# Performance work log

Measured on AMD Instinct MI355X. Metric: run time of the kernel, lower is better.

The kernel has to match this reference:

```python
import jax, jax.numpy as jnp
import numpy as np

B, C_IN, H, W = 8, 768, 64, 64
C_OUT = 768
C_QK = C_OUT // 8   # 96
C_V = C_OUT // 8    # 96


def setup_inputs() -> dict:
    key = jax.random.key(0)
    k0, k1, k2, k3, k4 = jax.random.split(key, 5)
    scale = 0.05
    return {
        "x": jax.random.normal(k0, (B, C_IN, H, W), jnp.float32),
        "Wq": jax.random.normal(k1, (C_QK, C_IN), jnp.float32) * scale,
        "Wk": jax.random.normal(k2, (C_QK, C_IN), jnp.float32) * scale,
        "Wv": jax.random.normal(k3, (C_V, C_IN), jnp.float32) * scale,
        "Wlast": jax.random.normal(k4, (C_OUT, C_V), jnp.float32) * scale,
        "gamma": jnp.ones((1,), jnp.float32),
    }


def reference(x, Wq, Wk, Wv, Wlast, gamma):
    # 1x1 convs == channel contractions; produce channels-last [B, H, W, C]
    q = jnp.einsum('bchw,oc->bhwo', x, Wq)   # [B, H, W, Cqk]
    k = jnp.einsum('bchw,oc->bhwo', x, Wk)   # [B, H, W, Cqk]
    v = jnp.einsum('bchw,oc->bhwo', x, Wv)   # [B, H, W, Cv]

    b, h, w, cq = q.shape
    L = h * w
    qf = q.reshape(b, L, cq)
    kf = k.reshape(b, L, cq)
    vf = v.reshape(b, L, v.shape[-1])

    # Unscaled full softmax attention over all spatial positions (batched).
    scores = jnp.einsum('bqc,bkc->bqk', qf, kf)        # [B, L, L]
    beta = jax.nn.softmax(scores, axis=-1)
    out = jnp.einsum('bqk,bkc->bqc', beta, vf)          # [B, L, Cv]
    out = out.reshape(b, h, w, -1)

    # last 1x1 conv (Cv -> C_OUT), scale by gamma, residual add
    y = jnp.einsum('bhwc,oc->bohw', out, Wlast)         # [B, C_OUT, H, W]
    return gamma[0] * y + x
```

## Files before the change

kernel.cpp:

```cpp
#include <hip/hip_runtime.h>

#define NB    8
#define CIN   768
#define LSP   4096
#define DD    96
#define COUT_ 768

typedef __attribute__((ext_vector_type(4))) float f32x4;
typedef __attribute__((ext_vector_type(8))) __bf16 bf16x8;
typedef __attribute__((ext_vector_type(8))) unsigned short us8;
typedef __attribute__((ext_vector_type(4))) unsigned short us4;

static __device__ __forceinline__ unsigned short f2bf(float f){
  union{float f; unsigned u;} v; v.f=f;
  unsigned r = v.u + 0x7FFFu + ((v.u>>16)&1u);
  return (unsigned short)(r>>16);
}
static __device__ __forceinline__ float bf2f(unsigned short s){
  union{unsigned u; float f;} v; v.u=((unsigned)s)<<16; return v.f;
}
static __device__ __forceinline__ unsigned fbits(float f){
  union{float f; unsigned u;} v; v.f=f; return v.u;
}
static __device__ __forceinline__ unsigned pack2(float lo, float hi){
  return __builtin_amdgcn_perm(fbits(hi), fbits(lo), 0x07060302u);
}
static __device__ __forceinline__ f32x4 mfma16(us8 a, us8 b, f32x4 c){
  union UA{us8 u; bf16x8 b;};
  UA A; A.u=a; UA B; B.u=b;
  return __builtin_amdgcn_mfma_f32_16x16x32_bf16(A.b, B.b, c, 0, 0, 0);
}

__global__ __launch_bounds__(256) void prep_w(
    const float* __restrict__ Wq, const float* __restrict__ Wk,
    const float* __restrict__ Wv, const float* __restrict__ Wl,
    unsigned short* __restrict__ wqh, unsigned short* __restrict__ wql,
    unsigned short* __restrict__ wkh, unsigned short* __restrict__ wkl,
    unsigned short* __restrict__ wvb, unsigned short* __restrict__ wlb){
  int i = blockIdx.x*256 + threadIdx.x;
  if (i < 96*768){
    float q = Wq[i]; unsigned short h = f2bf(q); wqh[i]=h; wql[i]=f2bf(q - bf2f(h));
    float k = Wk[i]; h = f2bf(k); wkh[i]=h; wkl[i]=f2bf(k - bf2f(h));
    wvb[i] = f2bf(Wv[i]);
    wlb[i] = f2bf(Wl[i]);
  }
}

__global__ __launch_bounds__(256) void proj_qkv(const float* __restrict__ x,
    const unsigned short* __restrict__ wqh, const unsigned short* __restrict__ wql,
    const unsigned short* __restrict__ wkh, const unsigned short* __restrict__ wkl,
    const unsigned short* __restrict__ wvb,
    unsigned short* __restrict__ qh, unsigned short* __restrict__ ql,
    unsigned short* __restrict__ kh, unsigned short* __restrict__ kl,
    unsigned short* __restrict__ vt){
  __shared__ __attribute__((aligned(16))) unsigned short xt_h[64*40];
  __shared__ __attribute__((aligned(16))) unsigned short xt_l[64*40];
  __shared__ __attribute__((aligned(16))) unsigned short swq_h[96*40];
  __shared__ __attribute__((aligned(16))) unsigned short swq_l[96*40];
  __shared__ __attribute__((aligned(16))) unsigned short swk_h[96*40];
  __shared__ __attribute__((aligned(16))) unsigned short swk_l[96*40];
  __shared__ __attribute__((aligned(16))) unsigned short swv [96*40];

  const int t = threadIdx.x;
  const int b = blockIdx.y;
  const int l0 = blockIdx.x*64;
  const int w = t>>6, lane = t&63, m16 = lane&15, quad = lane>>4;

  f32x4 zz = {0.f,0.f,0.f,0.f};
  f32x4 accq[6], acck[6], accv[6];
  #pragma unroll
  for (int i=0;i<6;i++){ accq[i]=zz; acck[i]=zz; accv[i]=zz; }

  const float* xb = x + (size_t)b*CIN*LSP;
  const int ci = t>>3, lj = (t&7)*8;

  #pragma unroll 1
  for (int cc=0; cc<24; ++cc){
    const int c0 = cc*32;
    __syncthreads();
    {
      const float* src = xb + (size_t)(c0+ci)*LSP + l0 + lj;
      f32x4 v0 = *(const f32x4*)src;
      f32x4 v1 = *(const f32x4*)(src+4);
      #pragma unroll
      for (int j=0;j<4;j++){
        float f = v0[j]; unsigned short h=f2bf(f);
        xt_h[(lj+j)*40+ci]=h; xt_l[(lj+j)*40+ci]=f2bf(f-bf2f(h));
      }
      #pragma unroll
      for (int j=0;j<4;j++){
        float f = v1[j]; unsigned short h=f2bf(f);
        xt_h[(lj+4+j)*40+ci]=h; xt_l[(lj+4+j)*40+ci]=f2bf(f-bf2f(h));
      }
    }
    for (int u=t; u<384; u+=256){
      const int o = u>>2, sg = (u&3)*8;
      const int g = o*CIN + c0 + sg;
      const int d = o*40 + sg;
      *(us8*)&swq_h[d] = *(const us8*)&wqh[g];
      *(us8*)&swq_l[d] = *(const us8*)&wql[g];
      *(us8*)&swk_h[d] = *(const us8*)&wkh[g];
      *(us8*)&swk_l[d] = *(const us8*)&wkl[g];
      *(us8*)&swv [d]  = *(const us8*)&wvb[g];
    }
    __syncthreads();

    const int lrow = w*16 + m16;
    us8 axh = *(const us8*)&xt_h[lrow*40 + quad*8];
    us8 axl = *(const us8*)&xt_l[lrow*40 + quad*8];
    #pragma unroll
    for (int nt=0; nt<6; ++nt){
      const int wr = (nt*16 + m16)*40 + quad*8;
      us8 bh = *(const us8*)&swq_h[wr];
      us8 bl = *(const us8*)&swq_l[wr];
      accq[nt] = mfma16(axh, bh, accq[nt]);
      accq[nt] = mfma16(axh, bl, accq[nt]);
      accq[nt] = mfma16(axl, bh, accq[nt]);
      bh = *(const us8*)&swk_h[wr];
      bl = *(const us8*)&swk_l[wr];
      acck[nt] = mfma16(axh, bh, acck[nt]);
      acck[nt] = mfma16(axh, bl, acck[nt]);
      acck[nt] = mfma16(axl, bh, acck[nt]);
      us8 av = *(const us8*)&swv[wr];
      accv[nt] = mfma16(av, axh, accv[nt]);
    }
  }
  #pragma unroll
  for (int nt=0; nt<6; ++nt){
    #pragma unroll
    for (int r=0; r<4; ++r){
      const int l = l0 + w*16 + quad*4 + r;
      const int o = nt*16 + m16;
      size_t qi = ((size_t)b*LSP + l)*DD + o;
      float fq = accq[nt][r];
      unsigned short h = f2bf(fq);
      qh[qi]=h; ql[qi]=f2bf(fq - bf2f(h));
      float fk = acck[nt][r];
      h = f2bf(fk);
      kh[qi]=h; kl[qi]=f2bf(fk - bf2f(h));
      const int vo = nt*16 + quad*4 + r;
      const int vl = l0 + w*16 + m16;
      vt[((size_t)b*DD + vo)*LSP + vl] = f2bf(accv[nt][r]);
    }
  }
}

__global__ __launch_bounds__(256, 2) void flash_attn3(
    const unsigned short* __restrict__ qh, const unsigned short* __restrict__ ql,
    const unsigned short* __restrict__ kh, const unsigned short* __restrict__ kl,
    const unsigned short* __restrict__ vt,
    unsigned short* __restrict__ U, float* __restrict__ Ms, float* __restrict__ Ls){
  __shared__ __attribute__((aligned(16))) unsigned short sk_h[64*96];
  __shared__ __attribute__((aligned(16))) unsigned short sk_l[64*96];
  __shared__ __attribute__((aligned(16))) unsigned short sv  [96*72];

  const int bid = blockIdx.x;
  const int b   = bid & 7;
  const int qt  = (bid >> 3) & 31;
  const int sp  = bid >> 8;
  const int l0  = qt*128;
  const int t = threadIdx.x;
  const int w = t>>6, lane = t&63, m16 = lane&15, quad = lane>>4;

  us8 bqh[2][3], bql[2][3];
  #pragma unroll
  for (int g=0; g<2; ++g){
    const int lq = l0 + w*32 + g*16 + m16;
    size_t qo = ((size_t)b*LSP + lq)*DD;
    #pragma unroll
    for (int ks=0;ks<3;ks++){
      bqh[g][ks] = *(const us8*)&qh[qo + ks*32 + quad*8];
      bql[g][ks] = *(const us8*)&ql[qo + ks*32 + quad*8];
    }
  }

  const int krow = t>>2, kc = (t&3);
  const int kg_off = krow*DD + kc*24;
  const int ksw    = krow*96 + kc*24;
  const int vd = t>>3, vc = t&7;
  const int vg_off = vd*LSP + vc*8;
  const int sigb = 32*((vc>>2)&1) + 16*(vc&1) + 4*((vc>>1)&1);
  const int vw = vd*72 + sigb;

  f32x4 zz = {0.f,0.f,0.f,0.f};
  f32x4 accO[2][6];
  #pragma unroll
  for (int g=0;g<2;g++)
    #pragma unroll
    for (int i=0;i<6;i++) accO[g][i]=zz;
  float mr[2] = {-3.0e38f, -3.0e38f}, lr[2] = {0.f, 0.f};

  const unsigned short* kh_it = kh + ((size_t)b*LSP + sp*2048)*DD;
  const unsigned short* kl_it = kl + ((size_t)b*LSP + sp*2048)*DD;
  const unsigned short* vt_it = vt + (size_t)b*DD*LSP + sp*2048;

  us8 rh[3], rl[3], rv[3];
  #pragma unroll
  for (int j=0;j<3;j++){
    rh[j] = *(const us8*)(kh_it + kg_off + j*8);
    rl[j] = *(const us8*)(kl_it + kg_off + j*8);
    rv[j] = *(const us8*)(vt_it + vg_off + j*32*LSP);
  }

  #pragma unroll 1
  for (int kt=0; kt<32; ++kt){
    __syncthreads();
    #pragma unroll
    for (int j=0;j<3;j++){
      *(us8*)&sk_h[ksw + j*8] = rh[j];
      *(us8*)&sk_l[ksw + j*8] = rl[j];
      union { us8 v; us4 h[2]; } u; u.v = rv[j];
      *(us4*)&sv[vw + j*32*72]     = u.h[0];
      *(us4*)&sv[vw + j*32*72 + 8] = u.h[1];
    }
    kh_it += 64*DD; kl_it += 64*DD; vt_it += 64;
    if (kt < 31){
      #pragma unroll
      for (int j=0;j<3;j++){
        rh[j] = *(const us8*)(kh_it + kg_off + j*8);
        rl[j] = *(const us8*)(kl_it + kg_off + j*8);
        rv[j] = *(const us8*)(vt_it + vg_off + j*32*LSP);
      }
    }
    __syncthreads();

    f32x4 s[2][4];
    #pragma unroll
    for (int nt=0; nt<4; ++nt){
      s[0][nt]=zz; s[1][nt]=zz;
      const int kr = (nt*16+m16)*96 + quad*8;
      #pragma unroll
      for (int ks=0; ks<3; ++ks){
        us8 ah = *(const us8*)&sk_h[kr + ks*32];
        us8 al = *(const us8*)&sk_l[kr + ks*32];
        #pragma unroll
        for (int g=0; g<2; ++g){
          s[g][nt] = mfma16(ah, bqh[g][ks], s[g][nt]);
          s[g][nt] = mfma16(ah, bql[g][ks], s[g][nt]);
          s[g][nt] = mfma16(al, bqh[g][ks], s[g][nt]);
        }
      }
    }

    us8 bp[2][2];
    #pragma unroll
    for (int g=0; g<2; ++g){
      float tm = s[g][0][0];
      #pragma unroll
      for (int nt=0;nt<4;nt++){
        #pragma unroll
        for (int r=0;r<4;r++) tm = fmaxf(tm, s[g][nt][r]);
      }
      tm = fmaxf(tm, __shfl_xor(tm, 16));
      tm = fmaxf(tm, __shfl_xor(tm, 32));
      float mn = fmaxf(mr[g], tm);
      float al = __expf(mr[g] - mn);
      mr[g] = mn;
      float p[4][4];
      float su = 0.f;
      #pragma unroll
      for (int nt=0;nt<4;nt++){
        #pragma unroll
        for (int r=0;r<4;r++){ p[nt][r] = __expf(s[g][nt][r] - mn); su += p[nt][r]; }
      }
      su += __shfl_xor(su, 16);
      su += __shfl_xor(su, 32);
      lr[g] = lr[g]*al + su;
      #pragma unroll
      for (int dt=0;dt<6;dt++){
        #pragma unroll
        for (int r=0;r<4;r++) accO[g][dt][r] *= al;
      }
      #pragma unroll
      for (int k2=0;k2<2;k2++){
        union {unsigned u[4]; us8 v;} pb;
        pb.u[0] = pack2(p[2*k2][0],   p[2*k2][1]);
        pb.u[1] = pack2(p[2*k2][2],   p[2*k2][3]);
        pb.u[2] = pack2(p[2*k2+1][0], p[2*k2+1][1]);
        pb.u[3] = pack2(p[2*k2+1][2], p[2*k2+1][3]);
        bp[g][k2] = pb.v;
      }
    }

    #pragma unroll
    for (int k2=0;k2<2;k2++){
      #pragma unroll
      for (int dt=0;dt<6;dt++){
        us8 av = *(const us8*)&sv[(dt*16+m16)*72 + k2*32 + quad*8];
        accO[0][dt] = mfma16(av, bp[0][k2], accO[0][dt]);
        accO[1][dt] = mfma16(av, bp[1][k2], accO[1][dt]);
      }
    }
  }

  #pragma unroll
  for (int g=0; g<2; ++g){
    const int q = l0 + w*32 + g*16 + m16;
    size_t ub = (((size_t)sp*NB + b)*LSP + q)*DD;
    #pragma unroll
    for (int dt=0;dt<6;dt++){
      #pragma unroll
      for (int r=0;r<4;r++)
        U[ub + dt*16 + quad*4 + r] = f2bf(accO[g][dt][r]);
    }
    if (quad == 0){
      size_t mi = ((size_t)sp*NB + b)*LSP + q;
      Ms[mi] = mr[g];
      Ls[mi] = lr[g];
    }
  }
}

__global__ __launch_bounds__(256) void merge2(
    const unsigned short* __restrict__ U, const float* __restrict__ Ms,
    const float* __restrict__ Ls, unsigned short* __restrict__ ob){
  int idx = blockIdx.x*256 + threadIdx.x;
  int row = idx / 12, ch = idx % 12;
  float m0 = Ms[row],          m1 = Ms[NB*LSP + row];
  float l0 = Ls[row],          l1 = Ls[NB*LSP + row];
  float M  = fmaxf(m0, m1);
  float w0 = __expf(m0 - M), w1 = __expf(m1 - M);
  float inv = 1.0f/(w0*l0 + w1*l1);
  w0 *= inv; w1 *= inv;
  us8 u0 = *(const us8*)&U[(size_t)row*DD + ch*8];
  us8 u1 = *(const us8*)&U[(size_t)NB*LSP*DD + (size_t)row*DD + ch*8];
  us8 o;
  #pragma unroll
  for (int j=0;j<8;j++) o[j] = f2bf(w0*bf2f(u0[j]) + w1*bf2f(u1[j]));
  *(us8*)&ob[(size_t)row*DD + ch*8] = o;
}

__global__ __launch_bounds__(256) void lastproj(
    const unsigned short* __restrict__ outb, const unsigned short* __restrict__ wlb,
    const float* __restrict__ x, const float* __restrict__ gamma, float* __restrict__ y){
  __shared__ __attribute__((aligned(16))) unsigned short so [64*104];
  __shared__ __attribute__((aligned(16))) unsigned short swl[64*104];
  const int t = threadIdx.x;
  const int bid = blockIdx.x;
  const int b  = bid & 7;
  const int r2 = bid >> 3;
  const int o0 = (r2 % 12)*64;
  const int l0 = (r2 / 12)*64;
  const int srow = t>>2, sseg = (t&3)*24;
  {
    size_t og = ((size_t)b*LSP + l0 + srow)*DD + sseg;
    size_t wg = (size_t)(o0 + srow)*DD + sseg;
    #pragma unroll
    for (int j=0;j<3;j++){
      *(us8*)&so [srow*104 + sseg + j*8] = *(const us8*)&outb[og + j*8];
      *(us8*)&swl[srow*104 + sseg + j*8] = *(const us8*)&wlb[wg + j*8];
    }
  }
  __syncthreads();
  const int w = t>>6, lane = t&63, m16 = lane&15, quad = lane>>4;
  us8 aw[3];
  #pragma unroll
  for (int ks=0;ks<3;ks++) aw[ks] = *(const us8*)&swl[(w*16+m16)*104 + ks*32 + quad*8];
  f32x4 zz = {0.f,0.f,0.f,0.f};
  f32x4 acc[4];
  #pragma unroll
  for (int i=0;i<4;i++) acc[i]=zz;
  #pragma unroll
  for (int nt=0;nt<4;nt++){
    const int orow = (nt*16+m16)*104;
    #pragma unroll
    for (int ks=0;ks<3;ks++){
      us8 bo = *(const us8*)&so[orow + ks*32 + quad*8];
      acc[nt] = mfma16(aw[ks], bo, acc[nt]);
    }
  }
  const float g = gamma[0];
  #pragma unroll
  for (int nt=0;nt<4;nt++){
    #pragma unroll
    for (int r=0;r<4;r++){
      const int o = o0 + w*16 + quad*4 + r;
      const int l = l0 + nt*16 + m16;
      size_t idx = ((size_t)b*COUT_ + o)*LSP + l;
      y[idx] = g*acc[nt][r] + x[idx];
    }
  }
}

extern "C" void kernel_launch(void* const* d_in, const int* in_sizes, int n_in,
                              void* d_out, int out_size, void* d_ws, size_t ws_size,
                              hipStream_t stream){
  (void)in_sizes; (void)n_in; (void)out_size; (void)ws_size;
  const float* x  = (const float*)d_in[0];
  const float* Wq = (const float*)d_in[1];
  const float* Wk = (const float*)d_in[2];
  const float* Wv = (const float*)d_in[3];
  const float* Wl = (const float*)d_in[4];
  const float* gm = (const float*)d_in[5];
  float* y = (float*)d_out;

  char* p = (char*)d_ws;
  const size_t big = (size_t)NB*LSP*DD*2;
  unsigned short* qh  = (unsigned short*)p; p += big;
  unsigned short* ql_ = (unsigned short*)p; p += big;
  unsigned short* kh  = (unsigned short*)p; p += big;
  unsigned short* kl  = (unsigned short*)p; p += big;
  unsigned short* vt  = (unsigned short*)p; p += big;
  unsigned short* ob  = (unsigned short*)p; p += big;
  unsigned short* Ubuf = (unsigned short*)p; p += 2*big;
  float* Ms = (float*)p; p += (size_t)2*NB*LSP*sizeof(float);
  float* Ls = (float*)p; p += (size_t)2*NB*LSP*sizeof(float);
  const size_t wsz = (size_t)96*768*2;
  unsigned short* wqh=(unsigned short*)p; p+=wsz;
  unsigned short* wql=(unsigned short*)p; p+=wsz;
  unsigned short* wkh=(unsigned short*)p; p+=wsz;
  unsigned short* wkl=(unsigned short*)p; p+=wsz;
  unsigned short* wvb=(unsigned short*)p; p+=wsz;
  unsigned short* wlb=(unsigned short*)p; p+=wsz;

  prep_w    <<<dim3(288),  dim3(256), 0, stream>>>(Wq,Wk,Wv,Wl,wqh,wql,wkh,wkl,wvb,wlb);
  proj_qkv  <<<dim3(64,8), dim3(256), 0, stream>>>(x,wqh,wql,wkh,wkl,wvb,qh,ql_,kh,kl,vt);
  flash_attn3<<<dim3(512), dim3(256), 0, stream>>>(qh,ql_,kh,kl,vt,Ubuf,Ms,Ls);
  merge2    <<<dim3(1536), dim3(256), 0, stream>>>(Ubuf,Ms,Ls,ob);
  lastproj  <<<dim3(6144), dim3(256), 0, stream>>>(ob,wlb,x,gm,y);
}
```

Measured before the change: 343.5 us.

## Split attention KV into four chunks and load x directly into registers

The flash attention kernel now splits keys into four 1024-wide chunks instead of two, launching 1024 blocks with a higher occupancy target, and the merge combines four partial results. The projection kernel drops the LDS transpose of x. Each lane reads x columns straight into registers, prefetched one chunk ahead, and Q is stored transposed to fit the new MFMA operand order. This trades extra partial-output traffic and merge work for better CU utilization and less LDS staging. It also adds strided scalar Q loads in the attention prologue.

```diff
diff --git a/kernel.cpp b/kernel.cpp
--- a/kernel.cpp
+++ b/kernel.cpp
@@ -46,20 +46,18 @@
   }
 }
 
-__global__ __launch_bounds__(256) void proj_qkv(const float* __restrict__ x,
+__global__ __launch_bounds__(256, 2) void proj_qkv2(const float* __restrict__ x,
     const unsigned short* __restrict__ wqh, const unsigned short* __restrict__ wql,
     const unsigned short* __restrict__ wkh, const unsigned short* __restrict__ wkl,
     const unsigned short* __restrict__ wvb,
-    unsigned short* __restrict__ qh, unsigned short* __restrict__ ql,
+    unsigned short* __restrict__ qth, unsigned short* __restrict__ qtl,
     unsigned short* __restrict__ kh, unsigned short* __restrict__ kl,
     unsigned short* __restrict__ vt){
-  __shared__ __attribute__((aligned(16))) unsigned short xt_h[64*40];
-  __shared__ __attribute__((aligned(16))) unsigned short xt_l[64*40];
-  __shared__ __attribute__((aligned(16))) unsigned short swq_h[96*40];
-  __shared__ __attribute__((aligned(16))) unsigned short swq_l[96*40];
-  __shared__ __attribute__((aligned(16))) unsigned short swk_h[96*40];
-  __shared__ __attribute__((aligned(16))) unsigned short swk_l[96*40];
-  __shared__ __attribute__((aligned(16))) unsigned short swv [96*40];
+  __shared__ __attribute__((aligned(16))) unsigned short swq_h[96*32];
+  __shared__ __attribute__((aligned(16))) unsigned short swq_l[96*32];
+  __shared__ __attribute__((aligned(16))) unsigned short swk_h[96*32];
+  __shared__ __attribute__((aligned(16))) unsigned short swk_l[96*32];
+  __shared__ __attribute__((aligned(16))) unsigned short swv [96*32];
 
   const int t = threadIdx.x;
   const int b = blockIdx.y;
@@ -71,32 +69,21 @@
   #pragma unroll
   for (int i=0;i<6;i++){ accq[i]=zz; acck[i]=zz; accv[i]=zz; }
 
-  const float* xb = x + (size_t)b*CIN*LSP;
-  const int ci = t>>3, lj = (t&7)*8;
+  const int lx = l0 + w*16 + m16;
+  const float* xp = x + (size_t)b*CIN*LSP + (size_t)(quad*8)*LSP + lx;
+
+  float xr[8];
+  #pragma unroll
+  for (int j=0;j<8;j++) xr[j] = xp[(size_t)j*LSP];
 
   #pragma unroll 1
   for (int cc=0; cc<24; ++cc){
     const int c0 = cc*32;
     __syncthreads();
-    {
-      const float* src = xb + (size_t)(c0+ci)*LSP + l0 + lj;
-      f32x4 v0 = *(const f32x4*)src;
-      f32x4 v1 = *(const f32x4*)(src+4);
-      #pragma unroll
-      for (int j=0;j<4;j++){
-        float f = v0[j]; unsigned short h=f2bf(f);
-        xt_h[(lj+j)*40+ci]=h; xt_l[(lj+j)*40+ci]=f2bf(f-bf2f(h));
-      }
-      #pragma unroll
-      for (int j=0;j<4;j++){
-        float f = v1[j]; unsigned short h=f2bf(f);
-        xt_h[(lj+4+j)*40+ci]=h; xt_l[(lj+4+j)*40+ci]=f2bf(f-bf2f(h));
-      }
-    }
     for (int u=t; u<384; u+=256){
       const int o = u>>2, sg = (u&3)*8;
       const int g = o*CIN + c0 + sg;
-      const int d = o*40 + sg;
+      const int d = o*32 + sg;
       *(us8*)&swq_h[d] = *(const us8*)&wqh[g];
       *(us8*)&swq_l[d] = *(const us8*)&wql[g];
       *(us8*)&swk_h[d] = *(const us8*)&wkh[g];
@@ -105,48 +92,61 @@
     }
     __syncthreads();
 
-    const int lrow = w*16 + m16;
-    us8 axh = *(const us8*)&xt_h[lrow*40 + quad*8];
-    us8 axl = *(const us8*)&xt_l[lrow*40 + quad*8];
+    us8 bxh, bxl;
+    #pragma unroll
+    for (int j=0;j<8;j++){
+      float f = xr[j];
+      unsigned short h = f2bf(f);
+      bxh[j] = h;
+      bxl[j] = f2bf(f - bf2f(h));
+    }
+    if (cc < 23){
+      const float* xn = xp + (size_t)(c0+32)*LSP;
+      #pragma unroll
+      for (int j=0;j<8;j++) xr[j] = xn[(size_t)j*LSP];
+    }
+
     #pragma unroll
     for (int nt=0; nt<6; ++nt){
-      const int wr = (nt*16 + m16)*40 + quad*8;
-      us8 bh = *(const us8*)&swq_h[wr];
-      us8 bl = *(const us8*)&swq_l[wr];
-      accq[nt] = mfma16(axh, bh, accq[nt]);
-      accq[nt] = mfma16(axh, bl, accq[nt]);
-      accq[nt] = mfma16(axl, bh, accq[nt]);
-      bh = *(const us8*)&swk_h[wr];
-      bl = *(const us8*)&swk_l[wr];
-      acck[nt] = mfma16(axh, bh, acck[nt]);
-      acck[nt] = mfma16(axh, bl, acck[nt]);
-      acck[nt] = mfma16(axl, bh, acck[nt]);
-      us8 av = *(const us8*)&swv[wr];
-      accv[nt] = mfma16(av, axh, accv[nt]);
-    }
-  }
+      const int base = (nt*16 + m16)*32 + quad*8;
+      us8 ah = *(const us8*)&swq_h[base];
+      us8 al = *(const us8*)&swq_l[base];
+      accq[nt] = mfma16(ah, bxh, accq[nt]);
+      accq[nt] = mfma16(ah, bxl, accq[nt]);
+      accq[nt] = mfma16(al, bxh, accq[nt]);
+      ah = *(const us8*)&swk_h[base];
+      al = *(const us8*)&swk_l[base];
+      acck[nt] = mfma16(ah, bxh, acck[nt]);
+      acck[nt] = mfma16(ah, bxl, acck[nt]);
+      acck[nt] = mfma16(al, bxh, acck[nt]);
+      us8 av = *(const us8*)&swv[base];
+      accv[nt] = mfma16(av, bxh, accv[nt]);
+    }
+  }
+
+  const int l = l0 + w*16 + m16;
   #pragma unroll
   for (int nt=0; nt<6; ++nt){
     #pragma unroll
     for (int r=0; r<4; ++r){
-      const int l = l0 + w*16 + quad*4 + r;
-      const int o = nt*16 + m16;
-      size_t qi = ((size_t)b*LSP + l)*DD + o;
+      const int o = nt*16 + quad*4 + r;
       float fq = accq[nt][r];
       unsigned short h = f2bf(fq);
-      qh[qi]=h; ql[qi]=f2bf(fq - bf2f(h));
+      size_t qi = ((size_t)b*DD + o)*LSP + l;
+      qth[qi] = h;
+      qtl[qi] = f2bf(fq - bf2f(h));
       float fk = acck[nt][r];
       h = f2bf(fk);
-      kh[qi]=h; kl[qi]=f2bf(fk - bf2f(h));
-      const int vo = nt*16 + quad*4 + r;
-      const int vl = l0 + w*16 + m16;
-      vt[((size_t)b*DD + vo)*LSP + vl] = f2bf(accv[nt][r]);
-    }
-  }
-}
-
-__global__ __launch_bounds__(256, 2) void flash_attn3(
-    const unsigned short* __restrict__ qh, const unsigned short* __restrict__ ql,
+      size_t ki = ((size_t)b*LSP + l)*DD + o;
+      kh[ki] = h;
+      kl[ki] = f2bf(fk - bf2f(h));
+      vt[((size_t)b*DD + o)*LSP + l] = f2bf(accv[nt][r]);
+    }
+  }
+}
+
+__global__ __launch_bounds__(256, 4) void flash_attn4(
+    const unsigned short* __restrict__ qth, const unsigned short* __restrict__ qtl,
     const unsigned short* __restrict__ kh, const unsigned short* __restrict__ kl,
     const unsigned short* __restrict__ vt,
     unsigned short* __restrict__ U, float* __restrict__ Ms, float* __restrict__ Ls){
@@ -166,11 +166,17 @@
   #pragma unroll
   for (int g=0; g<2; ++g){
     const int lq = l0 + w*32 + g*16 + m16;
-    size_t qo = ((size_t)b*LSP + lq)*DD;
     #pragma unroll
     for (int ks=0;ks<3;ks++){
-      bqh[g][ks] = *(const us8*)&qh[qo + ks*32 + quad*8];
-      bql[g][ks] = *(const us8*)&ql[qo + ks*32 + quad*8];
+      union {unsigned short s[8]; us8 v;} th, tl;
+      #pragma unroll
+      for (int j=0;j<8;j++){
+        size_t a = ((size_t)b*DD + ks*32 + quad*8 + j)*LSP + lq;
+        th.s[j] = qth[a];
+        tl.s[j] = qtl[a];
+      }
+      bqh[g][ks] = th.v;
+      bql[g][ks] = tl.v;
     }
   }
 
@@ -190,9 +196,9 @@
     for (int i=0;i<6;i++) accO[g][i]=zz;
   float mr[2] = {-3.0e38f, -3.0e38f}, lr[2] = {0.f, 0.f};
 
-  const unsigned short* kh_it = kh + ((size_t)b*LSP + sp*2048)*DD;
-  const unsigned short* kl_it = kl + ((size_t)b*LSP + sp*2048)*DD;
-  const unsigned short* vt_it = vt + (size_t)b*DD*LSP + sp*2048;
+  const unsigned short* kh_it = kh + ((size_t)b*LSP + sp*1024)*DD;
+  const unsigned short* kl_it = kl + ((size_t)b*LSP + sp*1024)*DD;
+  const unsigned short* vt_it = vt + (size_t)b*DD*LSP + sp*1024;
 
   us8 rh[3], rl[3], rv[3];
   #pragma unroll
@@ -203,7 +209,7 @@
   }
 
   #pragma unroll 1
-  for (int kt=0; kt<32; ++kt){
+  for (int kt=0; kt<16; ++kt){
     __syncthreads();
     #pragma unroll
     for (int j=0;j<3;j++){
@@ -214,7 +220,7 @@
       *(us4*)&sv[vw + j*32*72 + 8] = u.h[1];
     }
     kh_it += 64*DD; kl_it += 64*DD; vt_it += 64;
-    if (kt < 31){
+    if (kt < 15){
       #pragma unroll
       for (int j=0;j<3;j++){
         rh[j] = *(const us8*)(kh_it + kg_off + j*8);
@@ -311,23 +317,31 @@
   }
 }
 
-__global__ __launch_bounds__(256) void merge2(
+__global__ __launch_bounds__(256) void merge4(
     const unsigned short* __restrict__ U, const float* __restrict__ Ms,
     const float* __restrict__ Ls, unsigned short* __restrict__ ob){
   int idx = blockIdx.x*256 + threadIdx.x;
   int row = idx / 12, ch = idx % 12;
-  float m0 = Ms[row],          m1 = Ms[NB*LSP + row];
-  float l0 = Ls[row],          l1 = Ls[NB*LSP + row];
-  float M  = fmaxf(m0, m1);
-  float w0 = __expf(m0 - M), w1 = __expf(m1 - M);
-  float inv = 1.0f/(w0*l0 + w1*l1);
-  w0 *= inv; w1 *= inv;
-  us8 u0 = *(const us8*)&U[(size_t)row*DD + ch*8];
-  us8 u1 = *(const us8*)&U[(size_t)NB*LSP*DD + (size_t)row*DD + ch*8];
-  us8 o;
-  #pragma unroll
-  for (int j=0;j<8;j++) o[j] = f2bf(w0*bf2f(u0[j]) + w1*bf2f(u1[j]));
-  *(us8*)&ob[(size_t)row*DD + ch*8] = o;
+  float m[4], lsum[4];
+  #pragma unroll
+  for (int i=0;i<4;i++){ m[i] = Ms[(size_t)i*NB*LSP + row]; lsum[i] = Ls[(size_t)i*NB*LSP + row]; }
+  float M = fmaxf(fmaxf(m[0],m[1]), fmaxf(m[2],m[3]));
+  float wgt[4], den = 0.f;
+  #pragma unroll
+  for (int i=0;i<4;i++){ wgt[i] = __expf(m[i]-M); den += wgt[i]*lsum[i]; }
+  float inv = 1.0f/den;
+  float o[8] = {0,0,0,0,0,0,0,0};
+  #pragma unroll
+  for (int i=0;i<4;i++){
+    float wi = wgt[i]*inv;
+    us8 u = *(const us8*)&U[(size_t)i*NB*LSP*DD + (size_t)row*DD + ch*8];
+    #pragma unroll
+    for (int j=0;j<8;j++) o[j] += wi*bf2f(u[j]);
+  }
+  us8 ov;
+  #pragma unroll
+  for (int j=0;j<8;j++) ov[j] = f2bf(o[j]);
+  *(us8*)&ob[(size_t)row*DD + ch*8] = ov;
 }
 
 __global__ __launch_bounds__(256) void lastproj(
@@ -396,15 +410,15 @@
 
   char* p = (char*)d_ws;
   const size_t big = (size_t)NB*LSP*DD*2;
-  unsigned short* qh  = (unsigned short*)p; p += big;
-  unsigned short* ql_ = (unsigned short*)p; p += big;
+  unsigned short* qth = (unsigned short*)p; p += big;
+  unsigned short* qtl = (unsigned short*)p; p += big;
   unsigned short* kh  = (unsigned short*)p; p += big;
   unsigned short* kl  = (unsigned short*)p; p += big;
   unsigned short* vt  = (unsigned short*)p; p += big;
   unsigned short* ob  = (unsigned short*)p; p += big;
-  unsigned short* Ubuf = (unsigned short*)p; p += 2*big;
-  float* Ms = (float*)p; p += (size_t)2*NB*LSP*sizeof(float);
-  float* Ls = (float*)p; p += (size_t)2*NB*LSP*sizeof(float);
+  unsigned short* Ubuf = (unsigned short*)p; p += 4*big;
+  float* Ms = (float*)p; p += (size_t)4*NB*LSP*sizeof(float);
+  float* Ls = (float*)p; p += (size_t)4*NB*LSP*sizeof(float);
   const size_t wsz = (size_t)96*768*2;
   unsigned short* wqh=(unsigned short*)p; p+=wsz;
   unsigned short* wql=(unsigned short*)p; p+=wsz;
@@ -414,8 +428,8 @@
   unsigned short* wlb=(unsigned short*)p; p+=wsz;
 
   prep_w    <<<dim3(288),  dim3(256), 0, stream>>>(Wq,Wk,Wv,Wl,wqh,wql,wkh,wkl,wvb,wlb);
-  proj_qkv  <<<dim3(64,8), dim3(256), 0, stream>>>(x,wqh,wql,wkh,wkl,wvb,qh,ql_,kh,kl,vt);
-  flash_attn3<<<dim3(512), dim3(256), 0, stream>>>(qh,ql_,kh,kl,vt,Ubuf,Ms,Ls);
-  merge2    <<<dim3(1536), dim3(256), 0, stream>>>(Ubuf,Ms,Ls,ob);
+  proj_qkv2 <<<dim3(64,8), dim3(256), 0, stream>>>(x,wqh,wql,wkh,wkl,wvb,qth,qtl,kh,kl,vt);
+  flash_attn4<<<dim3(1024),dim3(256), 0, stream>>>(qth,qtl,kh,kl,vt,Ubuf,Ms,Ls);
+  merge4    <<<dim3(1536), dim3(256), 0, stream>>>(Ubuf,Ms,Ls,ob);
   lastproj  <<<dim3(6144), dim3(256), 0, stream>>>(ob,wlb,x,gm,y);
 }
```

New measurement: 642.1 us. 86.9% more time.
